# Kernel optimization log

Measured on AMD Instinct MI355X. Metric: run time of the kernel, lower is better.

Reference implementation:

```python
import jax, jax.numpy as jnp
import numpy as np

B, J, HID, INTER, NL = 4096, 16, 128, 64, 4
NEG = -9.0e15
EDGES = [(0,1),(1,2),(2,3),(0,4),(4,5),(5,6),(0,7),(7,8),(8,9),(8,10),(10,11),(11,12),(8,13),(13,14),(14,15)]
GROUPED = [0,7,1,4,2,5,3,6,8,10,9,13,11,14,12,15]  # flattened nodes_group


def _adjacency_nonzeros():
    A = np.zeros((J, J), np.float32)
    for i, j in EDGES:
        A[i, j] = 1.0
        A[j, i] = 1.0
    A += np.eye(J, dtype=np.float32)
    rows, cols = np.nonzero(A)  # row-major, matches torch adj[mask] = e fill order
    return rows.astype(np.int32), cols.astype(np.int32)


def setup_inputs() -> dict:
    key = jax.random.key(0)
    ks = iter(jax.random.split(key, 64))
    rn = lambda shape, s: jax.random.normal(next(ks), shape, jnp.float32) * s
    rows, cols = _adjacency_nonzeros()
    nnz = rows.shape[0]  # 46
    inp = dict(
        x=jax.random.normal(next(ks), (B, J, 2), jnp.float32),
        # input SemGraphConv (2 -> HID) + its BatchNorm
        gc_in_W=rn((2, 2, HID), 0.7), gc_in_e=1.0 + rn((nnz,), 0.3), gc_in_b=rn((HID,), 0.05),
        bn_in_g=1.0 + rn((HID,), 0.05), bn_in_b=rn((HID,), 0.05),
        # 4 residual blocks x 2 graph convs (HID -> HID)
        W_res=rn((2 * NL, 2, HID, HID), 0.08), e_res=1.0 + rn((2 * NL, nnz), 0.3),
        b_res=rn((2 * NL, HID), 0.05),
        bng_res=1.0 + rn((2 * NL, HID), 0.05), bnb_res=rn((2 * NL, HID), 0.05),
        # 5 GraphNonLocal blocks (1 after input + 1 per residual block)
        nl_g_w=rn((NL + 1, INTER, HID), 0.08), nl_g_b=rn((NL + 1, INTER), 0.05),
        nl_t_w=rn((NL + 1, INTER, HID), 0.08), nl_t_b=rn((NL + 1, INTER), 0.05),
        nl_p_w=rn((NL + 1, INTER, HID), 0.08), nl_p_b=rn((NL + 1, INTER), 0.05),
        nl_cp_w=rn((NL + 1, 2 * INTER), 0.08),  # concat_project 1x1 conv, no bias
        nl_W_w=rn((NL + 1, HID, INTER), 0.08), nl_W_b=rn((NL + 1, HID), 0.05),
        nl_bn_g=1.0 + rn((NL + 1, HID), 0.05), nl_bn_b=rn((NL + 1, HID), 0.05),
        # output SemGraphConv (HID -> 3)
        gc_out_W=rn((2, HID, 3), 0.08), gc_out_e=1.0 + rn((nnz,), 0.3), gc_out_b=rn((3,), 0.05),
        # integer constants
        mask_rows=jnp.asarray(rows), mask_cols=jnp.asarray(cols),
        grouped_order=jnp.asarray(GROUPED, jnp.int32),
        restored_order=jnp.asarray(np.argsort(GROUPED), jnp.int32),
    )
    return inp


def reference(x, gc_in_W, gc_in_e, gc_in_b, bn_in_g, bn_in_b,
              W_res, e_res, b_res, bng_res, bnb_res,
              nl_g_w, nl_g_b, nl_t_w, nl_t_b, nl_p_w, nl_p_b,
              nl_cp_w, nl_W_w, nl_W_b, nl_bn_g, nl_bn_b,
              gc_out_W, gc_out_e, gc_out_b,
              mask_rows, mask_cols, grouped_order, restored_order):
    eye = jnp.eye(J, dtype=x.dtype)

    def gconv(h, W, e, b):
        # h: [B, J, F]
        h0 = jnp.einsum('bjf,fo->bjo', h, W[0])
        h1 = jnp.einsum('bjf,fo->bjo', h, W[1])
        logits = jnp.full((J, J), NEG, h.dtype).at[mask_rows, mask_cols].set(e)
        adj = jax.nn.softmax(logits, axis=1)
        diag = jnp.diagonal(adj)                     # adj*I picks diagonal scaling
        off = adj * (1.0 - eye)
        return diag[None, :, None] * h0 + jnp.einsum('ij,bjo->bio', off, h1) + b

    def bn(h, g, bta, axes):
        # training-mode BatchNorm (biased variance), per-channel
        m = h.mean(axes, keepdims=True)
        v = h.var(axes, keepdims=True)
        return (h - m) * jax.lax.rsqrt(v + 1e-5) * g + bta

    def graph_conv(h, W, e, b, gm, gb):
        h = gconv(h, W, e, b)
        h = bn(h, gm[None, None, :], gb[None, None, :], (0, 1))
        return jax.nn.relu(h)

    def nonlocal_block(h, i):
        xo = h[:, grouped_order]          # [B, J, C] regroup joints
        xc = xo.transpose(0, 2, 1)        # [B, C, J]
        conv = lambda w, bb: jnp.einsum('oc,bcj->boj', w, xc) + bb[None, :, None]
        pool = lambda t: t.reshape(B, INTER, J // 2, 2).max(-1)   # MaxPool1d(k=2)
        gx = pool(conv(nl_g_w[i], nl_g_b[i]))                     # [B, I, J/2]
        th = conv(nl_t_w[i], nl_t_b[i])                           # [B, I, J]
        ph = pool(conv(nl_p_w[i], nl_p_b[i]))                     # [B, I, J/2]
        wt, wp = nl_cp_w[i][:INTER], nl_cp_w[i][INTER:]
        # concat_project 1x1 conv over concat(theta,phi) decomposes into a sum
        f = jax.nn.relu(jnp.einsum('bch,c->bh', th, wt)[:, :, None]
                        + jnp.einsum('bcw,c->bw', ph, wp)[:, None, :])  # [B, J, J/2]
        f = f / (J // 2)
        y = jnp.einsum('bhw,bcw->bch', f, gx)                     # [B, I, J]
        Wy = jnp.einsum('oc,bch->boh', nl_W_w[i], y) + nl_W_b[i][None, :, None]
        Wy = bn(Wy, nl_bn_g[i][None, :, None], nl_bn_b[i][None, :, None], (0, 2))
        z = Wy + xc
        return z.transpose(0, 2, 1)[:, restored_order]

    out = graph_conv(x, gc_in_W, gc_in_e, gc_in_b, bn_in_g, bn_in_b)
    out = nonlocal_block(out, 0)
    for i in range(NL):
        res = out
        out = graph_conv(out, W_res[2 * i], e_res[2 * i], b_res[2 * i], bng_res[2 * i], bnb_res[2 * i])
        out = graph_conv(out, W_res[2 * i + 1], e_res[2 * i + 1], b_res[2 * i + 1], bng_res[2 * i + 1], bnb_res[2 * i + 1])
        out = res + out
        out = nonlocal_block(out, i + 1)
    return gconv(out, gc_out_W, gc_out_e, gc_out_b)  # [B, J, 3]
```

## Files before the change

### kernel.cpp

```cpp
#include <hip/hip_runtime.h>

#define B 4096
#define J 16
#define HID 128
#define INTER 64
#define NLAYERS 4
#define NEGV -9000000000000000.0f
#define ELEMS ((size_t)B*16*128)
#define NREP 16
#define SLOT 4096

typedef __attribute__((ext_vector_type(8))) short short8;
typedef __attribute__((ext_vector_type(4))) float f32x4;

static __device__ __forceinline__ unsigned short f2bf(float x) {
    unsigned u = __float_as_uint(x);
    unsigned r = u + 0x7fffu + ((u >> 16) & 1u);
    return (unsigned short)(r >> 16);
}
static __device__ __forceinline__ void splitbf(float x, unsigned short& h, unsigned short& l) {
    h = f2bf(x);
    float hf = __uint_as_float((unsigned)h << 16);
    l = f2bf(x - hf);
}
static __device__ __forceinline__ void splitbf4(float4 v, uint2& hh, uint2& ll) {
    unsigned short h0,l0,h1,l1,h2,l2,h3,l3;
    splitbf(v.x,h0,l0); splitbf(v.y,h1,l1); splitbf(v.z,h2,l2); splitbf(v.w,h3,l3);
    hh = make_uint2((unsigned)h0 | ((unsigned)h1<<16), (unsigned)h2 | ((unsigned)h3<<16));
    ll = make_uint2((unsigned)l0 | ((unsigned)l1<<16), (unsigned)l2 | ((unsigned)l3<<16));
}
static __device__ __forceinline__ f32x4 mfma16(short8 a, short8 b, f32x4 c) {
    return __builtin_amdgcn_mfma_f32_16x16x32_bf16(a, b, c, 0, 0, 0);
}
static __device__ __forceinline__ f32x4 mfma_split(short8 ah, short8 al,
                                                   short8 bh, short8 bl, f32x4 acc) {
    acc = mfma16(ah, bh, acc);
    acc = mfma16(ah, bl, acc);
    acc = mfma16(al, bh, acc);
    return acc;
}
static __device__ __forceinline__ float bfpair(unsigned short h, unsigned short l) {
    return __uint_as_float((unsigned)h << 16) + __uint_as_float((unsigned)l << 16);
}

__global__ void adj_kernel(const float* __restrict__ e_in,
                           const float* __restrict__ e_res,
                           const float* __restrict__ e_out,
                           const int* __restrict__ rows,
                           const int* __restrict__ cols, int nnz,
                           float* __restrict__ off_all,
                           float* __restrict__ diag_all) {
    int m = blockIdx.x;
    int i = threadIdx.x;
    const float* e = (m == 0) ? e_in : (m <= 8) ? e_res + (size_t)(m - 1) * nnz : e_out;
    float l[16];
    for (int j = 0; j < 16; j++) l[j] = NEGV;
    for (int k = 0; k < nnz; k++)
        if (rows[k] == i) l[cols[k]] = e[k];
    float mx = l[0];
    for (int j = 1; j < 16; j++) mx = fmaxf(mx, l[j]);
    float ex[16], s = 0.f;
    for (int j = 0; j < 16; j++) { ex[j] = expf(l[j] - mx); s += ex[j]; }
    float inv = 1.f / s;
    for (int j = 0; j < 16; j++) {
        float a = ex[j] * inv;
        if (j == i) { diag_all[m * 16 + i] = a; a = 0.f; }
        off_all[m * 256 + i * 16 + j] = a;
    }
}

#define WB_N   262144
#define NLW_N  122880
#define NLWW_N 40960
__global__ void prep_w_kernel(const float* __restrict__ W_res,
                              const float* __restrict__ g_w, const float* __restrict__ t_w,
                              const float* __restrict__ p_w, const float* __restrict__ W_w,
                              unsigned short* __restrict__ Wbh, unsigned short* __restrict__ Wbl,
                              unsigned short* __restrict__ nlwh, unsigned short* __restrict__ nlwl,
                              unsigned short* __restrict__ nlWh, unsigned short* __restrict__ nlWl) {
    int i = blockIdx.x * 256 + threadIdx.x;
    unsigned short h, l;
    if (i < WB_N) {
        int lay = i >> 15, rem = i & 32767, n = rem >> 8, k = rem & 255;
        int d = k >> 7, f = k & 127;
        splitbf(W_res[(((lay << 1) | d) * 128 + f) * 128 + n], h, l);
        Wbh[i] = h; Wbl[i] = l;
    } else if (i < WB_N + NLW_N) {
        int j = i - WB_N;
        int lay = j / 24576, r2 = j % 24576;
        int conv = r2 >> 13, oc = r2 & 8191;
        const float* src = conv == 0 ? g_w : conv == 1 ? t_w : p_w;
        splitbf(src[lay * 8192 + oc], h, l);
        nlwh[j] = h; nlwl[j] = l;
    } else if (i < WB_N + NLW_N + NLWW_N) {
        int j = i - WB_N - NLW_N;
        splitbf(W_w[j], h, l);
        nlWh[j] = h; nlWl[j] = l;
    }
}

__global__ void prep_vt_kernel(const float* __restrict__ t_w, const float* __restrict__ t_b,
                               const float* __restrict__ cp_w,
                               float* __restrict__ vt, float* __restrict__ ct) {
    int l = blockIdx.x, c = threadIdx.x;
    float s = 0.f;
    for (int c2 = 0; c2 < 64; c2++)
        s += cp_w[l * 128 + c2] * t_w[(l * 64 + c2) * 128 + c];
    vt[l * 128 + c] = s;
    if (c == 0) {
        float s2 = 0.f;
        for (int c2 = 0; c2 < 64; c2++) s2 += cp_w[l * 128 + c2] * t_b[l * 64 + c2];
        ct[l] = s2;
    }
}

__global__ __launch_bounds__(256) void gconv_in_kernel(
        const float* __restrict__ x, const float* __restrict__ W,
        const float* __restrict__ bias, const float* __restrict__ off,
        const float* __restrict__ diag, float* __restrict__ out,
        float* __restrict__ stats_out) {
    __shared__ float xs[16][2];
    __shared__ float gs[16][2];
    __shared__ float red[512];
    int b = blockIdx.x, t = threadIdx.x;
    if (t < 32) xs[t >> 1][t & 1] = x[b * 32 + t];
    __syncthreads();
    if (t < 32) {
        int i = t >> 1, f = t & 1;
        float g = 0.f;
        #pragma unroll
        for (int j = 0; j < 16; j++) g += off[i * 16 + j] * xs[j][f];
        gs[i][f] = g;
    }
    __syncthreads();
    int o = t & 127;
    float w00 = W[o], w01 = W[128 + o], w10 = W[256 + o], w11 = W[384 + o], bo = bias[o];
    float s = 0.f, q = 0.f;
    for (int idx = t; idx < 2048; idx += 256) {
        int i = idx >> 7;
        float v = diag[i] * (xs[i][0] * w00 + xs[i][1] * w01)
                + gs[i][0] * w10 + gs[i][1] * w11 + bo;
        out[(size_t)b * 2048 + idx] = v;
        s += v; q += v * v;
    }
    red[t] = s; red[256 + t] = q;
    __syncthreads();
    float* so = stats_out + (b & (NREP - 1)) * 256;
    if (t < 128) {
        atomicAdd(&so[t], red[t] + red[t + 128]);
        atomicAdd(&so[128 + t], red[256 + t] + red[256 + t + 128]);
    }
}

__global__ __launch_bounds__(256) void gconv_mfma_kernel(
        const float* src, const float* wy,
        const float* __restrict__ stats_in,
        const float* __restrict__ bn_g, const float* __restrict__ bn_b,
        const int* __restrict__ restored, float* zdst,
        const unsigned short* __restrict__ Wbh,
        const unsigned short* __restrict__ Wbl,
        const float* __restrict__ bias,
        const float* __restrict__ off, const float* __restrict__ diag,
        float* dst, float* __restrict__ stats_out) {
    __shared__ float hraw[16][132];
    __shared__ __align__(16) unsigned short ksh[16][264];
    __shared__ __align__(16) unsigned short ksl[16][264];
    __shared__ float offs[256];
    __shared__ float diags[16];
    int t = threadIdx.x;
    offs[t] = off[t];
    if (t < 16) diags[t] = diag[t];
    float* hrawf = &hraw[0][0];
    {
        float ssum = 0.f;
        #pragma unroll
        for (int rr = 0; rr < NREP; rr++) ssum += stats_in[rr * 256 + t];
        hrawf[t] = ssum;
    }
    int c4 = (4 * t) & 127;
    int r0 = t >> 5;
    int ro0 = 0, ro1 = 0;
    if (wy) { ro0 = restored[r0]; ro1 = restored[r0 + 8]; }
    int b0 = blockIdx.x;
    const float4* src4 = (const float4*)src;
    const float4* wy4  = (const float4*)wy;
    float4 sv0 = src4[(size_t)b0 * 512 + t];
    float4 sv1 = src4[(size_t)b0 * 512 + 256 + t];
    float4 wv0 = make_float4(0,0,0,0), wv1 = make_float4(0,0,0,0);
    if (wy) {
        wv0 = wy4[(size_t)b0 * 512 + ro0 * 32 + (c4 >> 2)];
        wv1 = wy4[(size_t)b0 * 512 + ro1 * 32 + (c4 >> 2)];
    }
    __syncthreads();
    float4 m4, sc4, bb4;
    {
        const float K = 1.f / 65536.f;
        float4 g4 = *(const float4*)&bn_g[c4];
        bb4 = *(const float4*)&bn_b[c4];
        float m0 = hrawf[c4]     * K, m1 = hrawf[c4 + 1] * K;
        float m2 = hrawf[c4 + 2] * K, m3 = hrawf[c4 + 3] * K;
        float i0 = rsqrtf(hrawf[128 + c4]     * K - m0 * m0 + 1e-5f);
        float i1 = rsqrtf(hrawf[128 + c4 + 1] * K - m1 * m1 + 1e-5f);
        float i2 = rsqrtf(hrawf[128 + c4 + 2] * K - m2 * m2 + 1e-5f);
        float i3 = rsqrtf(hrawf[128 + c4 + 3] * K - m3 * m3 + 1e-5f);
        m4 = make_float4(m0, m1, m2, m3);
        sc4 = make_float4(i0 * g4.x, i1 * g4.y, i2 * g4.z, i3 * g4.w);
    }
    __syncthreads();
    int wv_ = t >> 6, lane = t & 63;
    int mn = lane & 15, kq = (lane >> 4) << 3, qr = (lane >> 4) << 2;

    for (int s = 0; s < 2; s++) {
        int bb_ = blockIdx.x + s * 2048;
        {
            float4 v = sv0;
            if (wy) {
                v.x += (wv0.x - m4.x) * sc4.x + bb4.x;
                v.y += (wv0.y - m4.y) * sc4.y + bb4.y;
                v.z += (wv0.z - m4.z) * sc4.z + bb4.z;
                v.w += (wv0.w - m4.w) * sc4.w + bb4.w;
                ((float4*)zdst)[(size_t)bb_ * 512 + t] = v;
            } else {
                v.x = fmaxf((v.x - m4.x) * sc4.x + bb4.x, 0.f);
                v.y = fmaxf((v.y - m4.y) * sc4.y + bb4.y, 0.f);
                v.z = fmaxf((v.z - m4.z) * sc4.z + bb4.z, 0.f);
                v.w = fmaxf((v.w - m4.w) * sc4.w + bb4.w, 0.f);
            }
            *(float4*)&hraw[r0][c4] = v;
            v = sv1;
            if (wy) {
                v.x += (wv1.x - m4.x) * sc4.x + bb4.x;
                v.y += (wv1.y - m4.y) * sc4.y + bb4.y;
                v.z += (wv1.z - m4.z) * sc4.z + bb4.z;
                v.w += (wv1.w - m4.w) * sc4.w + bb4.w;
                ((float4*)zdst)[(size_t)bb_ * 512 + 256 + t] = v;
            } else {
                v.x = fmaxf((v.x - m4.x) * sc4.x + bb4.x, 0.f);
                v.y = fmaxf((v.y - m4.y) * sc4.y + bb4.y, 0.f);
                v.z = fmaxf((v.z - m4.z) * sc4.z + bb4.z, 0.f);
                v.w = fmaxf((v.w - m4.w) * sc4.w + bb4.w, 0.f);
            }
            *(float4*)&hraw[r0 + 8][c4] = v;
        }
        if (s == 0) {
            int b1 = blockIdx.x + 2048;
            sv0 = src4[(size_t)b1 * 512 + t];
            sv1 = src4[(size_t)b1 * 512 + 256 + t];
            if (wy) {
                wv0 = wy4[(size_t)b1 * 512 + ro0 * 32 + (c4 >> 2)];
                wv1 = wy4[(size_t)b1 * 512 + ro1 * 32 + (c4 >> 2)];
            }
        }
        __syncthreads();
        for (int u = t; u < 512; u += 256) {
            int i = u >> 5, f4 = (u & 31) << 2;
            float4 hv = *(const float4*)&hraw[i][f4];
            float4 g = make_float4(0.f, 0.f, 0.f, 0.f);
            #pragma unroll
            for (int j = 0; j < 16; j++) {
                float w = offs[i * 16 + j];
                float4 hj = *(const float4*)&hraw[j][f4];
                g.x += w * hj.x; g.y += w * hj.y; g.z += w * hj.z; g.w += w * hj.w;
            }
            float d = diags[i];
            uint2 hh, ll;
            splitbf4(make_float4(d * hv.x, d * hv.y, d * hv.z, d * hv.w), hh, ll);
            *(uint2*)&ksh[i][f4] = hh;
            *(uint2*)&ksl[i][f4] = ll;
            splitbf4(g, hh, ll);
            *(uint2*)&ksh[i][128 + f4] = hh;
            *(uint2*)&ksl[i][128 + f4] = ll;
        }
        __syncthreads();
        int n0 = wv_ << 5;
        f32x4 acc0 = {0.f, 0.f, 0.f, 0.f}, acc1 = {0.f, 0.f, 0.f, 0.f};
        const unsigned short* wh0 = Wbh + (size_t)(n0 + mn) * 256 + kq;
        const unsigned short* wl0 = Wbl + (size_t)(n0 + mn) * 256 + kq;
        #pragma unroll
        for (int k = 0; k < 8; k++) {
            int k0 = k << 5;
            short8 ah = *(const short8*)&ksh[mn][k0 + kq];
            short8 al = *(const short8*)&ksl[mn][k0 + kq];
            acc0 = mfma_split(ah, al, *(const short8*)(wh0 + k0), *(const short8*)(wl0 + k0), acc0);
            acc1 = mfma_split(ah, al, *(const short8*)(wh0 + 4096 + k0), *(const short8*)(wl0 + 4096 + k0), acc1);
        }
        float bias0 = bias[n0 + mn], bias1 = bias[n0 + 16 + mn];
        float s0 = 0.f, q0 = 0.f, s1 = 0.f, q1 = 0.f;
        #pragma unroll
        for (int r = 0; r < 4; r++) {
            int row = qr + r;
            float v0 = acc0[r] + bias0;
            float v1 = acc1[r] + bias1;
            dst[(size_t)bb_ * 2048 + row * 128 + n0 + mn] = v0;
            dst[(size_t)bb_ * 2048 + row * 128 + n0 + 16 + mn] = v1;
            s0 += v0; q0 += v0 * v0; s1 += v1; q1 += v1 * v1;
        }
        s0 += __shfl_xor(s0, 16); s0 += __shfl_xor(s0, 32);
        q0 += __shfl_xor(q0, 16); q0 += __shfl_xor(q0, 32);
        s1 += __shfl_xor(s1, 16); s1 += __shfl_xor(s1, 32);
        q1 += __shfl_xor(q1, 16); q1 += __shfl_xor(q1, 32);
        float* so = stats_out + (bb_ & (NREP - 1)) * 256;
        if (lane < 16) {
            atomicAdd(&so[n0 + mn], s0);
            atomicAdd(&so[128 + n0 + mn], q0);
            atomicAdd(&so[n0 + 16 + mn], s1);
            atomicAdd(&so[128 + n0 + 16 + mn], q1);
        }
        if (s == 0) __syncthreads();
    }
}

#define CG(conv, o, j) cgbuf[((conv) * 64 + (o)) * 17 + (j)]
#define WYL(o, j)      cgbuf[(o) * 17 + (j)]
__global__ __launch_bounds__(256, 8) void nl_a_kernel(
        const float* tsrc, const float* __restrict__ stats_in,
        const float* __restrict__ bn_g, const float* __restrict__ bn_b,
        const float* res,
        const unsigned short* __restrict__ nlwh,
        const unsigned short* __restrict__ nlwl,
        const float* __restrict__ g_b, const float* __restrict__ p_b,
        const float* __restrict__ cpw,
        const float* __restrict__ vt, const float* __restrict__ ctp,
        const unsigned short* __restrict__ nlWh,
        const unsigned short* __restrict__ nlWl,
        const float* __restrict__ W_b,
        const int* __restrict__ restored,
        float* hdst, float* wydst, float* __restrict__ wst) {
    __shared__ __align__(16) unsigned short xch[16][136];
    __shared__ __align__(16) unsigned short xcl[16][136];
    __shared__ float cgbuf[2176];
    __shared__ float gx[64][9];
    __shared__ float tv[16], pv[8];
    __shared__ float vtl[128];
    __shared__ float redS[256];
    unsigned short (*ybh)[72] = (unsigned short (*)[72])&xch[0][0];
    unsigned short (*ybl)[72] = (unsigned short (*)[72])&xcl[0][0];
    int t = threadIdx.x, b = blockIdx.x;
    const float4* tsrc4 = (const float4*)tsrc;
    float4 sv0 = tsrc4[(size_t)b * 512 + t];
    float4 sv1 = tsrc4[(size_t)b * 512 + 256 + t];
    float4 rv0 = make_float4(0.f, 0.f, 0.f, 0.f), rv1 = rv0;
    if (res) {
        rv0 = ((const float4*)res)[(size_t)b * 512 + t];
        rv1 = ((const float4*)res)[(size_t)b * 512 + 256 + t];
    }
    {
        float ssum = 0.f;
        #pragma unroll
        for (int rr = 0; rr < NREP; rr++) ssum += stats_in[rr * 256 + t];
        redS[t] = ssum;
    }
    if (t < 128) vtl[t] = vt[t];
    int c4 = (4 * t) & 127;
    int r0 = t >> 5;
    int rg0 = restored[r0];
    int rg1 = restored[r0 + 8];
    __syncthreads();
    int w = t >> 6, lane = t & 63;
    int mn = lane & 15, kq = (lane >> 4) << 3, qr = (lane >> 4) << 2;
    float4 h0, h1;
    {
        const float K = 1.f / 65536.f;
        float4 g4 = *(const float4*)&bn_g[c4];
        float4 bb4 = *(const float4*)&bn_b[c4];
        float m0 = redS[c4] * K,       m1 = redS[c4 + 1] * K;
        float m2 = redS[c4 + 2] * K,   m3 = redS[c4 + 3] * K;
        float s0 = rsqrtf(redS[128 + c4]     * K - m0 * m0 + 1e-5f) * g4.x;
        float s1 = rsqrtf(redS[128 + c4 + 1] * K - m1 * m1 + 1e-5f) * g4.y;
        float s2 = rsqrtf(redS[128 + c4 + 2] * K - m2 * m2 + 1e-5f) * g4.z;
        float s3 = rsqrtf(redS[128 + c4 + 3] * K - m3 * m3 + 1e-5f) * g4.w;
        h0.x = fmaxf((sv0.x - m0) * s0 + bb4.x, 0.f) + rv0.x;
        h0.y = fmaxf((sv0.y - m1) * s1 + bb4.y, 0.f) + rv0.y;
        h0.z = fmaxf((sv0.z - m2) * s2 + bb4.z, 0.f) + rv0.z;
        h0.w = fmaxf((sv0.w - m3) * s3 + bb4.w, 0.f) + rv0.w;
        h1.x = fmaxf((sv1.x - m0) * s0 + bb4.x, 0.f) + rv1.x;
        h1.y = fmaxf((sv1.y - m1) * s1 + bb4.y, 0.f) + rv1.y;
        h1.z = fmaxf((sv1.z - m2) * s2 + bb4.z, 0.f) + rv1.z;
        h1.w = fmaxf((sv1.w - m3) * s3 + bb4.w, 0.f) + rv1.w;
        uint2 hh, ll;
        splitbf4(h0, hh, ll);
        *(uint2*)&xch[rg0][c4] = hh;
        *(uint2*)&xcl[rg0][c4] = ll;
        splitbf4(h1, hh, ll);
        *(uint2*)&xch[rg1][c4] = hh;
        *(uint2*)&xcl[rg1][c4] = ll;
    }
    __syncthreads();
    #pragma unroll
    for (int i = 0; i < 2; i++) {
        int tile = 2 * w + i;
        int conv = tile >> 2;
        int mt = tile & 3;
        int wbase = (conv == 0) ? 0 : 128;
        const unsigned short* aph = nlwh + (size_t)(wbase + mt * 16 + mn) * 128 + kq;
        const unsigned short* apl = nlwl + (size_t)(wbase + mt * 16 + mn) * 128 + kq;
        f32x4 acc = {0.f, 0.f, 0.f, 0.f};
        #pragma unroll
        for (int k = 0; k < 4; k++) {
            short8 bh = *(const short8*)&xch[mn][k * 32 + kq];
            short8 bl = *(const short8*)&xcl[mn][k * 32 + kq];
            acc = mfma_split(*(const short8*)(aph + k * 32), *(const short8*)(apl + k * 32),
                             bh, bl, acc);
        }
        const float* biasp = (conv == 0) ? g_b : p_b;
        #pragma unroll
        for (int r = 0; r < 4; r++) {
            int o = mt * 16 + qr + r;
            CG(conv, o, mn) = acc[r] + biasp[o];
        }
    }
    __syncthreads();
    {
        #pragma unroll
        for (int u2 = 0; u2 < 2; u2++) {
            int u = t + u2 * 256;
            int cc = u >> 3, w2 = u & 7;
            gx[cc][w2] = fmaxf(CG(0, cc, 2 * w2), CG(0, cc, 2 * w2 + 1));
        }
        if (t < 64) {
            int ch = t >> 3, w2 = t & 7;
            float ss = 0.f;
            for (int cc = ch * 8; cc < ch * 8 + 8; cc++)
                ss += fmaxf(CG(1, cc, 2 * w2), CG(1, cc, 2 * w2 + 1)) * cpw[64 + cc];
            ss += __shfl_xor(ss, 8);
            ss += __shfl_xor(ss, 16);
            ss += __shfl_xor(ss, 32);
            if (t < 8) pv[t] = ss;
        } else if (t < 128) {
            int u = t - 64, j = u & 15, ch = u >> 4;
            float ss = 0.f;
            int c0 = ch * 32;
            for (int cc = c0; cc < c0 + 32; cc += 2) {
                unsigned hh = *(const unsigned*)&xch[j][cc];
                unsigned ll = *(const unsigned*)&xcl[j][cc];
                float v0 = bfpair((unsigned short)hh, (unsigned short)ll);
                float v1 = bfpair((unsigned short)(hh >> 16), (unsigned short)(ll >> 16));
                ss += vtl[cc] * v0 + vtl[cc + 1] * v1;
            }
            ss += __shfl_xor(ss, 16);
            ss += __shfl_xor(ss, 32);
            if (u < 16) tv[u] = ss + ctp[0];
        }
    }
    __syncthreads();
    #pragma unroll
    for (int u2 = 0; u2 < 4; u2++) {
        int u = t + u2 * 256;
        int j = u >> 6, c = u & 63;
        float ss = 0.f;
        #pragma unroll
        for (int w2 = 0; w2 < 8; w2++)
            ss += fmaxf(tv[j] + pv[w2], 0.f) * gx[c][w2];
        unsigned short h2, l2;
        splitbf(ss * 0.125f, h2, l2);
        ybh[j][c] = h2; ybl[j][c] = l2;
    }
    __syncthreads();
    {
        short8 byh0 = *(const short8*)&ybh[mn][kq];
        short8 byh1 = *(const short8*)&ybh[mn][32 + kq];
        short8 byl0 = *(const short8*)&ybl[mn][kq];
        short8 byl1 = *(const short8*)&ybl[mn][32 + kq];
        #pragma unroll
        for (int i = 0; i < 2; i++) {
            int mt = 2 * w + i;
            const unsigned short* aph = nlWh + (size_t)(mt * 16 + mn) * 64 + kq;
            const unsigned short* apl = nlWl + (size_t)(mt * 16 + mn) * 64 + kq;
            f32x4 acc = {0.f, 0.f, 0.f, 0.f};
            acc = mfma_split(*(const short8*)aph, *(const short8*)apl, byh0, byl0, acc);
            acc = mfma_split(*(const short8*)(aph + 32), *(const short8*)(apl + 32), byh1, byl1, acc);
            #pragma unroll
            for (int r = 0; r < 4; r++) {
                int o = mt * 16 + qr + r;
                WYL(o, mn) = acc[r] + W_b[o];
            }
        }
    }
    __syncthreads();
    {
        int c = t & 127;
        float ss = 0.f, qq = 0.f;
        #pragma unroll
        for (int u2 = 0; u2 < 8; u2++) {
            int idx = t + u2 * 256;
            int j = idx >> 7;
            float v = WYL(c, j);
            wydst[(size_t)b * 2048 + idx] = v;
            ss += v; qq += v * v;
        }
        float* so = wst + (b & (NREP - 1)) * 256;
        atomicAdd(&so[c], ss);
        atomicAdd(&so[128 + c], qq);
        ((float4*)hdst)[(size_t)b * 512 + t] = h0;
        ((float4*)hdst)[(size_t)b * 512 + 256 + t] = h1;
    }
}

__global__ __launch_bounds__(256) void gconv_out_kernel(
        const float* __restrict__ h, const float* __restrict__ wy,
        const float* __restrict__ stats_in,
        const float* __restrict__ nlg, const float* __restrict__ nlb,
        const int* __restrict__ restored,
        const float* __restrict__ W,
        const float* __restrict__ bias, const float* __restrict__ off,
        const float* __restrict__ diag, float* __restrict__ out) {
    __shared__ float hs[16][132];
    __shared__ float gsv[16][132];
    __shared__ float offs[256];
    __shared__ float p0[48][4], p1[48][4];
    int b = blockIdx.x, t = threadIdx.x;
    offs[t] = off[t];
    float* hsf = &hs[0][0];
    {
        float ssum = 0.f;
        #pragma unroll
        for (int rr = 0; rr < NREP; rr++) ssum += stats_in[rr * 256 + t];
        hsf[t] = ssum;
    }
    __syncthreads();
    int c = t & 127;
    float mean, inv, bbv;
    {
        const float K = 1.f / 65536.f;
        mean = hsf[c] * K;
        float varv = hsf[128 + c] * K - mean * mean;
        inv = rsqrtf(varv + 1e-5f) * nlg[c];
        bbv = nlb[c];
    }
    __syncthreads();
    {
        for (int idx = t; idx < 2048; idx += 256) {
            int r = idx >> 7;
            float wval = wy[(size_t)b * 2048 + restored[r] * 128 + c];
            hs[r][c] = (wval - mean) * inv + bbv + h[(size_t)b * 2048 + idx];
        }
    }
    __syncthreads();
    for (int idx = t; idx < 2048; idx += 256) {
        int i = idx >> 7, f = idx & 127;
        float g = 0.f;
        #pragma unroll
        for (int j = 0; j < 16; j++) g += offs[i * 16 + j] * hs[j][f];
        gsv[i][f] = g;
    }
    __syncthreads();
    if (t < 192) {
        int oid = t >> 2, chunk = t & 3;
        int i = oid / 3, o = oid % 3;
        float a0 = 0.f, a1 = 0.f;
        int f0 = chunk * 32;
        for (int f = f0; f < f0 + 32; f++) {
            a0 += hs[i][f] * W[f * 3 + o];
            a1 += gsv[i][f] * W[384 + f * 3 + o];
        }
        p0[oid][chunk] = a0; p1[oid][chunk] = a1;
    }
    __syncthreads();
    if (t < 48) {
        int i = t / 3, o = t % 3;
        float a0 = p0[t][0] + p0[t][1] + p0[t][2] + p0[t][3];
        float a1 = p1[t][0] + p1[t][1] + p1[t][2] + p1[t][3];
        out[(size_t)b * 48 + t] = diag[i] * a0 + a1 + bias[o];
    }
}

extern "C" void kernel_launch(void* const* d_in, const int* in_sizes, int n_in,
                              void* d_out, int out_size, void* d_ws, size_t ws_size,
                              hipStream_t stream) {
    (void)n_in; (void)out_size; (void)ws_size;
    const float* x        = (const float*)d_in[0];
    const float* gc_in_W  = (const float*)d_in[1];
    const float* gc_in_e  = (const float*)d_in[2];
    const float* gc_in_b  = (const float*)d_in[3];
    const float* bn_in_g  = (const float*)d_in[4];
    const float* bn_in_b  = (const float*)d_in[5];
    const float* W_res    = (const float*)d_in[6];
    const float* e_res    = (const float*)d_in[7];
    const float* b_res    = (const float*)d_in[8];
    const float* bng_res  = (const float*)d_in[9];
    const float* bnb_res  = (const float*)d_in[10];
    const float* nl_g_w   = (const float*)d_in[11];
    const float* nl_g_b   = (const float*)d_in[12];
    const float* nl_t_w   = (const float*)d_in[13];
    const float* nl_t_b   = (const float*)d_in[14];
    const float* nl_p_w   = (const float*)d_in[15];
    const float* nl_p_b   = (const float*)d_in[16];
    const float* nl_cp_w  = (const float*)d_in[17];
    const float* nl_W_w   = (const float*)d_in[18];
    const float* nl_W_b   = (const float*)d_in[19];
    const float* nl_bn_g  = (const float*)d_in[20];
    const float* nl_bn_b  = (const float*)d_in[21];
    const float* gc_out_W = (const float*)d_in[22];
    const float* gc_out_e = (const float*)d_in[23];
    const float* gc_out_b = (const float*)d_in[24];
    const int*   mask_rows = (const int*)d_in[25];
    const int*   mask_cols = (const int*)d_in[26];
    const int*   restored  = (const int*)d_in[28];
    int nnz = in_sizes[2];

    float* ws       = (float*)d_ws;
    float* off_all  = ws;
    float* diag_all = ws + 2560;
    float* stats    = ws + 2720;
    float* vt       = ws + 63664;
    float* ct       = ws + 64304;
    unsigned short* Wbh  = (unsigned short*)(ws + 65536);
    unsigned short* Wbl  = Wbh + WB_N;
    unsigned short* nlwh = Wbl + WB_N;
    unsigned short* nlwl = nlwh + NLW_N;
    unsigned short* nlWh = nlwl + NLW_N;
    unsigned short* nlWl = nlWh + NLWW_N;
    float* Z = ws + 491520;
    float* T = Z + ELEMS;

    hipMemsetAsync(stats, 0, 14 * SLOT * sizeof(float), stream);
    adj_kernel<<<10, 16, 0, stream>>>(gc_in_e, e_res, gc_out_e, mask_rows, mask_cols,
                                      nnz, off_all, diag_all);
    prep_w_kernel<<<(WB_N + NLW_N + NLWW_N + 255) / 256, 256, 0, stream>>>(
        W_res, nl_g_w, nl_t_w, nl_p_w, nl_W_w, Wbh, Wbl, nlwh, nlwl, nlWh, nlWl);
    prep_vt_kernel<<<5, 128, 0, stream>>>(nl_t_w, nl_t_b, nl_cp_w, vt, ct);

    gconv_in_kernel<<<B, 256, 0, stream>>>(x, gc_in_W, gc_in_b, off_all, diag_all,
                                           T, stats);
    nl_a_kernel<<<B, 256, 0, stream>>>(T, stats, bn_in_g, bn_in_b, nullptr,
                                       nlwh, nlwl, nl_g_b, nl_p_b, nl_cp_w,
                                       vt, ct, nlWh, nlWl, nl_W_b, restored,
                                       Z, T, stats + SLOT);

    int sl = 1;
    for (int i = 0; i < NLAYERS; i++) {
        int l0 = 2 * i, l1 = 2 * i + 1, li = i + 1;
        gconv_mfma_kernel<<<2048, 256, 0, stream>>>(
            Z, T, stats + (size_t)sl * SLOT,
            nl_bn_g + i * 128, nl_bn_b + i * 128, restored, Z,
            Wbh + (size_t)l0 * 32768, Wbl + (size_t)l0 * 32768, b_res + l0 * 128,
            off_all + (1 + l0) * 256, diag_all + (1 + l0) * 16, T,
            stats + (size_t)(sl + 1) * SLOT);
        gconv_mfma_kernel<<<2048, 256, 0, stream>>>(
            T, nullptr, stats + (size_t)(sl + 1) * SLOT,
            bng_res + l0 * 128, bnb_res + l0 * 128, nullptr, nullptr,
            Wbh + (size_t)l1 * 32768, Wbl + (size_t)l1 * 32768, b_res + l1 * 128,
            off_all + (1 + l1) * 256, diag_all + (1 + l1) * 16, T,
            stats + (size_t)(sl + 2) * SLOT);
        nl_a_kernel<<<B, 256, 0, stream>>>(
            T, stats + (size_t)(sl + 2) * SLOT,
            bng_res + l1 * 128, bnb_res + l1 * 128, Z,
            nlwh + li * 24576, nlwl + li * 24576,
            nl_g_b + li * 64, nl_p_b + li * 64, nl_cp_w + li * 128,
            vt + li * 128, ct + li, nlWh + li * 8192, nlWl + li * 8192,
            nl_W_b + li * 128, restored, Z, T,
            stats + (size_t)(sl + 3) * SLOT);
        sl += 3;
    }
    gconv_out_kernel<<<B, 256, 0, stream>>>(Z, T, stats + (size_t)sl * SLOT,
                                            nl_bn_g + NLAYERS * 128, nl_bn_b + NLAYERS * 128,
                                            restored, gc_out_W, gc_out_b,
                                            off_all + 9 * 256, diag_all + 9 * 16,
                                            (float*)d_out);
}
```

Baseline: 893.2 us.

## Process two batch samples per block in nonlocal kernel with prefetch

The nonlocal kernel now runs with half as many blocks, and each block handles two samples (b0 and b0+2048). The next sample's inputs are prefetched from global memory while the first is being computed. The shared-memory stat reduction is done once per block, and the BN-statistics atomics are halved by accumulating across both samples. In exchange, per-block latency is longer and there are fewer blocks to hide stalls, and the loaded weight fragments are not reused across samples.

Result: slower. 969.4 us (+8.5%).

```diff
diff --git a/kernel.cpp b/kernel.cpp
--- a/kernel.cpp
+++ b/kernel.cpp
@@ -335,14 +335,15 @@
     __shared__ float redS[256];
     unsigned short (*ybh)[72] = (unsigned short (*)[72])&xch[0][0];
     unsigned short (*ybl)[72] = (unsigned short (*)[72])&xcl[0][0];
-    int t = threadIdx.x, b = blockIdx.x;
+    int t = threadIdx.x, b0 = blockIdx.x;
     const float4* tsrc4 = (const float4*)tsrc;
-    float4 sv0 = tsrc4[(size_t)b * 512 + t];
-    float4 sv1 = tsrc4[(size_t)b * 512 + 256 + t];
+    const float4* res4  = (const float4*)res;
+    float4 sv0 = tsrc4[(size_t)b0 * 512 + t];
+    float4 sv1 = tsrc4[(size_t)b0 * 512 + 256 + t];
     float4 rv0 = make_float4(0.f, 0.f, 0.f, 0.f), rv1 = rv0;
     if (res) {
-        rv0 = ((const float4*)res)[(size_t)b * 512 + t];
-        rv1 = ((const float4*)res)[(size_t)b * 512 + 256 + t];
+        rv0 = res4[(size_t)b0 * 512 + t];
+        rv1 = res4[(size_t)b0 * 512 + 256 + t];
     }
     {
         float ssum = 0.f;
@@ -358,141 +359,158 @@
     __syncthreads();
     int w = t >> 6, lane = t & 63;
     int mn = lane & 15, kq = (lane >> 4) << 3, qr = (lane >> 4) << 2;
-    float4 h0, h1;
-    {
-        const float K = 1.f / 65536.f;
-        float4 g4 = *(const float4*)&bn_g[c4];
-        float4 bb4 = *(const float4*)&bn_b[c4];
-        float m0 = redS[c4] * K,       m1 = redS[c4 + 1] * K;
-        float m2 = redS[c4 + 2] * K,   m3 = redS[c4 + 3] * K;
-        float s0 = rsqrtf(redS[128 + c4]     * K - m0 * m0 + 1e-5f) * g4.x;
-        float s1 = rsqrtf(redS[128 + c4 + 1] * K - m1 * m1 + 1e-5f) * g4.y;
-        float s2 = rsqrtf(redS[128 + c4 + 2] * K - m2 * m2 + 1e-5f) * g4.z;
-        float s3 = rsqrtf(redS[128 + c4 + 3] * K - m3 * m3 + 1e-5f) * g4.w;
-        h0.x = fmaxf((sv0.x - m0) * s0 + bb4.x, 0.f) + rv0.x;
-        h0.y = fmaxf((sv0.y - m1) * s1 + bb4.y, 0.f) + rv0.y;
-        h0.z = fmaxf((sv0.z - m2) * s2 + bb4.z, 0.f) + rv0.z;
-        h0.w = fmaxf((sv0.w - m3) * s3 + bb4.w, 0.f) + rv0.w;
-        h1.x = fmaxf((sv1.x - m0) * s0 + bb4.x, 0.f) + rv1.x;
-        h1.y = fmaxf((sv1.y - m1) * s1 + bb4.y, 0.f) + rv1.y;
-        h1.z = fmaxf((sv1.z - m2) * s2 + bb4.z, 0.f) + rv1.z;
-        h1.w = fmaxf((sv1.w - m3) * s3 + bb4.w, 0.f) + rv1.w;
-        uint2 hh, ll;
-        splitbf4(h0, hh, ll);
-        *(uint2*)&xch[rg0][c4] = hh;
-        *(uint2*)&xcl[rg0][c4] = ll;
-        splitbf4(h1, hh, ll);
-        *(uint2*)&xch[rg1][c4] = hh;
-        *(uint2*)&xcl[rg1][c4] = ll;
-    }
-    __syncthreads();
-    #pragma unroll
-    for (int i = 0; i < 2; i++) {
-        int tile = 2 * w + i;
-        int conv = tile >> 2;
-        int mt = tile & 3;
-        int wbase = (conv == 0) ? 0 : 128;
-        const unsigned short* aph = nlwh + (size_t)(wbase + mt * 16 + mn) * 128 + kq;
-        const unsigned short* apl = nlwl + (size_t)(wbase + mt * 16 + mn) * 128 + kq;
-        f32x4 acc = {0.f, 0.f, 0.f, 0.f};
-        #pragma unroll
-        for (int k = 0; k < 4; k++) {
-            short8 bh = *(const short8*)&xch[mn][k * 32 + kq];
-            short8 bl = *(const short8*)&xcl[mn][k * 32 + kq];
-            acc = mfma_split(*(const short8*)(aph + k * 32), *(const short8*)(apl + k * 32),
-                             bh, bl, acc);
-        }
-        const float* biasp = (conv == 0) ? g_b : p_b;
-        #pragma unroll
-        for (int r = 0; r < 4; r++) {
-            int o = mt * 16 + qr + r;
-            CG(conv, o, mn) = acc[r] + biasp[o];
-        }
-    }
-    __syncthreads();
-    {
-        #pragma unroll
-        for (int u2 = 0; u2 < 2; u2++) {
-            int u = t + u2 * 256;
-            int cc = u >> 3, w2 = u & 7;
-            gx[cc][w2] = fmaxf(CG(0, cc, 2 * w2), CG(0, cc, 2 * w2 + 1));
-        }
-        if (t < 64) {
-            int ch = t >> 3, w2 = t & 7;
-            float ss = 0.f;
-            for (int cc = ch * 8; cc < ch * 8 + 8; cc++)
-                ss += fmaxf(CG(1, cc, 2 * w2), CG(1, cc, 2 * w2 + 1)) * cpw[64 + cc];
-            ss += __shfl_xor(ss, 8);
-            ss += __shfl_xor(ss, 16);
-            ss += __shfl_xor(ss, 32);
-            if (t < 8) pv[t] = ss;
-        } else if (t < 128) {
-            int u = t - 64, j = u & 15, ch = u >> 4;
-            float ss = 0.f;
-            int c0 = ch * 32;
-            for (int cc = c0; cc < c0 + 32; cc += 2) {
-                unsigned hh = *(const unsigned*)&xch[j][cc];
-                unsigned ll = *(const unsigned*)&xcl[j][cc];
-                float v0 = bfpair((unsigned short)hh, (unsigned short)ll);
-                float v1 = bfpair((unsigned short)(hh >> 16), (unsigned short)(ll >> 16));
-                ss += vtl[cc] * v0 + vtl[cc + 1] * v1;
-            }
-            ss += __shfl_xor(ss, 16);
-            ss += __shfl_xor(ss, 32);
-            if (u < 16) tv[u] = ss + ctp[0];
-        }
-    }
-    __syncthreads();
-    #pragma unroll
-    for (int u2 = 0; u2 < 4; u2++) {
-        int u = t + u2 * 256;
-        int j = u >> 6, c = u & 63;
-        float ss = 0.f;
-        #pragma unroll
-        for (int w2 = 0; w2 < 8; w2++)
-            ss += fmaxf(tv[j] + pv[w2], 0.f) * gx[c][w2];
-        unsigned short h2, l2;
-        splitbf(ss * 0.125f, h2, l2);
-        ybh[j][c] = h2; ybl[j][c] = l2;
-    }
-    __syncthreads();
-    {
-        short8 byh0 = *(const short8*)&ybh[mn][kq];
-        short8 byh1 = *(const short8*)&ybh[mn][32 + kq];
-        short8 byl0 = *(const short8*)&ybl[mn][kq];
-        short8 byl1 = *(const short8*)&ybl[mn][32 + kq];
+    float sst = 0.f, qqt = 0.f;
+
+    for (int s = 0; s < 2; s++) {
+        int b = b0 + s * 2048;
+        {
+            const float K = 1.f / 65536.f;
+            float4 g4 = *(const float4*)&bn_g[c4];
+            float4 bb4 = *(const float4*)&bn_b[c4];
+            float m0 = redS[c4] * K,       m1 = redS[c4 + 1] * K;
+            float m2 = redS[c4 + 2] * K,   m3 = redS[c4 + 3] * K;
+            float s0 = rsqrtf(redS[128 + c4]     * K - m0 * m0 + 1e-5f) * g4.x;
+            float s1 = rsqrtf(redS[128 + c4 + 1] * K - m1 * m1 + 1e-5f) * g4.y;
+            float s2 = rsqrtf(redS[128 + c4 + 2] * K - m2 * m2 + 1e-5f) * g4.z;
+            float s3 = rsqrtf(redS[128 + c4 + 3] * K - m3 * m3 + 1e-5f) * g4.w;
+            float4 h0, h1;
+            h0.x = fmaxf((sv0.x - m0) * s0 + bb4.x, 0.f) + rv0.x;
+            h0.y = fmaxf((sv0.y - m1) * s1 + bb4.y, 0.f) + rv0.y;
+            h0.z = fmaxf((sv0.z - m2) * s2 + bb4.z, 0.f) + rv0.z;
+            h0.w = fmaxf((sv0.w - m3) * s3 + bb4.w, 0.f) + rv0.w;
+            h1.x = fmaxf((sv1.x - m0) * s0 + bb4.x, 0.f) + rv1.x;
+            h1.y = fmaxf((sv1.y - m1) * s1 + bb4.y, 0.f) + rv1.y;
+            h1.z = fmaxf((sv1.z - m2) * s2 + bb4.z, 0.f) + rv1.z;
+            h1.w = fmaxf((sv1.w - m3) * s3 + bb4.w, 0.f) + rv1.w;
+            ((float4*)hdst)[(size_t)b * 512 + t] = h0;
+            ((float4*)hdst)[(size_t)b * 512 + 256 + t] = h1;
+            uint2 hh, ll;
+            splitbf4(h0, hh, ll);
+            *(uint2*)&xch[rg0][c4] = hh;
+            *(uint2*)&xcl[rg0][c4] = ll;
+            splitbf4(h1, hh, ll);
+            *(uint2*)&xch[rg1][c4] = hh;
+            *(uint2*)&xcl[rg1][c4] = ll;
+        }
+        if (s == 0) {
+            int b1 = b0 + 2048;
+            sv0 = tsrc4[(size_t)b1 * 512 + t];
+            sv1 = tsrc4[(size_t)b1 * 512 + 256 + t];
+            if (res) {
+                rv0 = res4[(size_t)b1 * 512 + t];
+                rv1 = res4[(size_t)b1 * 512 + 256 + t];
+            }
+        }
+        __syncthreads();
         #pragma unroll
         for (int i = 0; i < 2; i++) {
-            int mt = 2 * w + i;
-            const unsigned short* aph = nlWh + (size_t)(mt * 16 + mn) * 64 + kq;
-            const unsigned short* apl = nlWl + (size_t)(mt * 16 + mn) * 64 + kq;
+            int tile = 2 * w + i;
+            int conv = tile >> 2;
+            int mt = tile & 3;
+            int wbase = (conv == 0) ? 0 : 128;
+            const unsigned short* aph = nlwh + (size_t)(wbase + mt * 16 + mn) * 128 + kq;
+            const unsigned short* apl = nlwl + (size_t)(wbase + mt * 16 + mn) * 128 + kq;
             f32x4 acc = {0.f, 0.f, 0.f, 0.f};
-            acc = mfma_split(*(const short8*)aph, *(const short8*)apl, byh0, byl0, acc);
-            acc = mfma_split(*(const short8*)(aph + 32), *(const short8*)(apl + 32), byh1, byl1, acc);
+            #pragma unroll
+            for (int k = 0; k < 4; k++) {
+                short8 bh = *(const short8*)&xch[mn][k * 32 + kq];
+                short8 bl = *(const short8*)&xcl[mn][k * 32 + kq];
+                acc = mfma_split(*(const short8*)(aph + k * 32), *(const short8*)(apl + k * 32),
+                                 bh, bl, acc);
+            }
+            const float* biasp = (conv == 0) ? g_b : p_b;
             #pragma unroll
             for (int r = 0; r < 4; r++) {
                 int o = mt * 16 + qr + r;
-                WYL(o, mn) = acc[r] + W_b[o];
-            }
-        }
-    }
-    __syncthreads();
+                CG(conv, o, mn) = acc[r] + biasp[o];
+            }
+        }
+        __syncthreads();
+        {
+            #pragma unroll
+            for (int u2 = 0; u2 < 2; u2++) {
+                int u = t + u2 * 256;
+                int cc = u >> 3, w2 = u & 7;
+                gx[cc][w2] = fmaxf(CG(0, cc, 2 * w2), CG(0, cc, 2 * w2 + 1));
+            }
+            if (t < 64) {
+                int ch = t >> 3, w2 = t & 7;
+                float ss = 0.f;
+                for (int cc = ch * 8; cc < ch * 8 + 8; cc++)
+                    ss += fmaxf(CG(1, cc, 2 * w2), CG(1, cc, 2 * w2 + 1)) * cpw[64 + cc];
+                ss += __shfl_xor(ss, 8);
+                ss += __shfl_xor(ss, 16);
+                ss += __shfl_xor(ss, 32);
+                if (t < 8) pv[t] = ss;
+            } else if (t < 128) {
+                int u = t - 64, j = u & 15, ch = u >> 4;
+                float ss = 0.f;
+                int c0 = ch * 32;
+                for (int cc = c0; cc < c0 + 32; cc += 2) {
+                    unsigned hh = *(const unsigned*)&xch[j][cc];
+                    unsigned ll = *(const unsigned*)&xcl[j][cc];
+                    float v0 = bfpair((unsigned short)hh, (unsigned short)ll);
+                    float v1 = bfpair((unsigned short)(hh >> 16), (unsigned short)(ll >> 16));
+                    ss += vtl[cc] * v0 + vtl[cc + 1] * v1;
+                }
+                ss += __shfl_xor(ss, 16);
+                ss += __shfl_xor(ss, 32);
+                if (u < 16) tv[u] = ss + ctp[0];
+            }
+        }
+        __syncthreads();
+        #pragma unroll
+        for (int u2 = 0; u2 < 4; u2++) {
+            int u = t + u2 * 256;
+            int j = u >> 6, c = u & 63;
+            float ss = 0.f;
+            #pragma unroll
+            for (int w2 = 0; w2 < 8; w2++)
+                ss += fmaxf(tv[j] + pv[w2], 0.f) * gx[c][w2];
+            unsigned short h2, l2;
+            splitbf(ss * 0.125f, h2, l2);
+            ybh[j][c] = h2; ybl[j][c] = l2;
+        }
+        __syncthreads();
+        {
+            short8 byh0 = *(const short8*)&ybh[mn][kq];
+            short8 byh1 = *(const short8*)&ybh[mn][32 + kq];
+            short8 byl0 = *(const short8*)&ybl[mn][kq];
+            short8 byl1 = *(const short8*)&ybl[mn][32 + kq];
+            #pragma unroll
+            for (int i = 0; i < 2; i++) {
+                int mt = 2 * w + i;
+                const unsigned short* aph = nlWh + (size_t)(mt * 16 + mn) * 64 + kq;
+                const unsigned short* apl = nlWl + (size_t)(mt * 16 + mn) * 64 + kq;
+                f32x4 acc = {0.f, 0.f, 0.f, 0.f};
+                acc = mfma_split(*(const short8*)aph, *(const short8*)apl, byh0, byl0, acc);
+                acc = mfma_split(*(const short8*)(aph + 32), *(const short8*)(apl + 32), byh1, byl1, acc);
+                #pragma unroll
+                for (int r = 0; r < 4; r++) {
+                    int o = mt * 16 + qr + r;
+                    WYL(o, mn) = acc[r] + W_b[o];
+                }
+            }
+        }
+        __syncthreads();
+        {
+            int c = t & 127;
+            #pragma unroll
+            for (int u2 = 0; u2 < 8; u2++) {
+                int idx = t + u2 * 256;
+                int j = idx >> 7;
+                float v = WYL(c, j);
+                wydst[(size_t)b * 2048 + idx] = v;
+                sst += v; qqt += v * v;
+            }
+        }
+        if (s == 0) __syncthreads();
+    }
     {
         int c = t & 127;
-        float ss = 0.f, qq = 0.f;
-        #pragma unroll
-        for (int u2 = 0; u2 < 8; u2++) {
-            int idx = t + u2 * 256;
-            int j = idx >> 7;
-            float v = WYL(c, j);
-            wydst[(size_t)b * 2048 + idx] = v;
-            ss += v; qq += v * v;
-        }
-        float* so = wst + (b & (NREP - 1)) * 256;
-        atomicAdd(&so[c], ss);
-        atomicAdd(&so[128 + c], qq);
-        ((float4*)hdst)[(size_t)b * 512 + t] = h0;
-        ((float4*)hdst)[(size_t)b * 512 + 256 + t] = h1;
+        float* so = wst + (b0 & (NREP - 1)) * 256;
+        atomicAdd(&so[c], sst);
+        atomicAdd(&so[128 + c], qqt);
     }
 }
 
@@ -622,10 +640,10 @@
 
     gconv_in_kernel<<<B, 256, 0, stream>>>(x, gc_in_W, gc_in_b, off_all, diag_all,
                                            T, stats);
-    nl_a_kernel<<<B, 256, 0, stream>>>(T, stats, bn_in_g, bn_in_b, nullptr,
-                                       nlwh, nlwl, nl_g_b, nl_p_b, nl_cp_w,
-                                       vt, ct, nlWh, nlWl, nl_W_b, restored,
-                                       Z, T, stats + SLOT);
+    nl_a_kernel<<<B / 2, 256, 0, stream>>>(T, stats, bn_in_g, bn_in_b, nullptr,
+                                           nlwh, nlwl, nl_g_b, nl_p_b, nl_cp_w,
+                                           vt, ct, nlWh, nlWl, nl_W_b, restored,
+                                           Z, T, stats + SLOT);
 
     int sl = 1;
     for (int i = 0; i < NLAYERS; i++) {
@@ -642,7 +660,7 @@
             Wbh + (size_t)l1 * 32768, Wbl + (size_t)l1 * 32768, b_res + l1 * 128,
             off_all + (1 + l1) * 256, diag_all + (1 + l1) * 16, T,
             stats + (size_t)(sl + 2) * SLOT);
-        nl_a_kernel<<<B, 256, 0, stream>>>(
+        nl_a_kernel<<<B / 2, 256, 0, stream>>>(
             T, stats + (size_t)(sl + 2) * SLOT,
             bng_res + l1 * 128, bnb_res + l1 * 128, Z,
             nlwh + li * 24576, nlwl + li * 24576,
```
